# Optimization experiments

Hardware: AMD Instinct MI355X
Metric: run time of the kernel (lower is better)

Reference implementation:

```python
import jax, jax.numpy as jnp
import numpy as np

B, T, D = 4, 2048, 512
H, DK = 8, 64  # n_head, d_kv; inner_dim = H*DK = 512


def setup_inputs() -> dict:
    key = jax.random.key(0)
    ks = jax.random.split(key, 6)
    s = 1.0 / np.sqrt(D)
    return {
        "x": jax.random.normal(ks[0], (B, T, D), dtype=jnp.float32),
        "mask": jnp.zeros((B, 1, 1, T), dtype=jnp.float32),
        "position_bias": jax.random.normal(ks[1], (1, H, T, T), dtype=jnp.float32),
        "Wq": jax.random.normal(ks[2], (D, D), dtype=jnp.float32) * s,
        "Wk": jax.random.normal(ks[3], (D, D), dtype=jnp.float32) * s,
        "Wv": jax.random.normal(ks[4], (D, D), dtype=jnp.float32) * s,
        "Wo": jax.random.normal(ks[5], (D, D), dtype=jnp.float32) * s,
    }


def reference(x, mask, position_bias, Wq, Wk, Wv, Wo):
    # Linear projections (torch nn.Linear: y = x @ W.T), split into heads.
    q = (x @ Wq.T).reshape(B, T, H, DK).transpose(0, 2, 1, 3)  # [B,H,T,DK]
    k = (x @ Wk.T).reshape(B, T, H, DK).transpose(0, 2, 1, 3)  # [B,H,S,DK]
    v = (x @ Wv.T).reshape(B, T, H, DK).transpose(0, 2, 1, 3)  # [B,H,S,DK]
    # T5: no 1/sqrt(d_k) scaling; additive position bias + mask before softmax.
    scores = jnp.einsum("bhtd,bhsd->bhts", q, k) + position_bias + mask
    attn = jax.nn.softmax(scores.astype(jnp.float32), axis=-1).astype(q.dtype)
    # dropout is identity at inference
    y = jnp.einsum("bhts,bhsd->bhtd", attn, v)  # [B,H,T,DK]
    y = y.transpose(0, 2, 1, 3).reshape(B, T, H * DK)
    return y @ Wo.T
```

## Files before the change

### kernel.cpp

```cpp
#include <hip/hip_runtime.h>
#include <stdint.h>

typedef unsigned short u16;
typedef __attribute__((ext_vector_type(8))) _Float16 half8;
typedef __attribute__((ext_vector_type(4))) float f32x4;

#define L2E 1.4426950408889634f

#define NTOK 8192
#define DIM  512
#define TT   2048

__device__ __forceinline__ u16 f2h(float f) {
  _Float16 h = (_Float16)f;
  return __builtin_bit_cast(u16, h);
}

__device__ __forceinline__ void async16(const void* g, void* l) {
  __builtin_amdgcn_global_load_lds(
      (const __attribute__((address_space(1))) unsigned int*)g,
      (__attribute__((address_space(3))) unsigned int*)l, 16, 0, 0);
}

__global__ __launch_bounds__(256) void k_convert(
    const float* __restrict__ x, const float* __restrict__ wq,
    const float* __restrict__ wk, const float* __restrict__ wv,
    const float* __restrict__ wo, u16* __restrict__ xb) {
  size_t i = ((size_t)blockIdx.x * 256 + threadIdx.x) * 8;
  const float* src;
  u16* dst;
  size_t off;
  if (i < 4194304) {
    src = x; dst = xb; off = i;
  } else {
    size_t j = i - 4194304;
    int w = (int)(j >> 18);
    off = j & 262143;
    src = (w == 0) ? wq : (w == 1) ? wk : (w == 2) ? wv : wo;
    dst = xb + 4194304 + (size_t)w * 262144;
  }
  float4 a = *(const float4*)(src + off);
  float4 b = *(const float4*)(src + off + 4);
  uint4 pk;
  pk.x = (unsigned)f2h(a.x) | ((unsigned)f2h(a.y) << 16);
  pk.y = (unsigned)f2h(a.z) | ((unsigned)f2h(a.w) << 16);
  pk.z = (unsigned)f2h(b.x) | ((unsigned)f2h(b.y) << 16);
  pk.w = (unsigned)f2h(b.z) | ((unsigned)f2h(b.w) << 16);
  *(uint4*)(dst + off) = pk;
}

template <bool VSWAP>
__global__ __launch_bounds__(256) void k_proj(
    const u16* __restrict__ A, const u16* __restrict__ Wb,
    u16* __restrict__ Db) {
  const int tid = threadIdx.x;
  const int wave = tid >> 6, lane = tid & 63;
  const int quad = lane >> 4, l16 = lane & 15;
  const int wr = wave >> 1, wc = wave & 1;
  const int m0 = blockIdx.x * 128, n0 = blockIdx.y * 128;

  const u16* W;
  u16* D;
  if (VSWAP) {
    W = Wb + 2 * 262144;
    D = Db + 2 * (size_t)4194304;
  } else {
    int z = blockIdx.z;
    W = Wb + (size_t)z * 262144;
    D = Db + (size_t)z * 4194304;
  }

  __shared__ __align__(16) u16 As[128 * 64];
  __shared__ __align__(16) u16 Bs[128 * 64];

  f32x4 acc[4][4];
  for (int rt = 0; rt < 4; ++rt)
    for (int ct = 0; ct < 4; ++ct) acc[rt][ct] = (f32x4){0.f, 0.f, 0.f, 0.f};

  for (int kb = 0; kb < 8; ++kb) {
    const int k0 = kb * 64;
    for (int r = 0; r < 4; ++r) {
      int cid = r * 256 + tid;
      int row = cid >> 3, cl = cid & 7, cg = cl ^ (row & 7);
      async16(A + (size_t)(m0 + row) * DIM + k0 + cg * 8,
              &As[(r * 256 + wave * 64) * 8]);
    }
    for (int r = 0; r < 4; ++r) {
      int cid = r * 256 + tid;
      int row = cid >> 3, cl = cid & 7, cg = cl ^ (row & 7);
      async16(W + (size_t)(n0 + row) * DIM + k0 + cg * 8,
              &Bs[(r * 256 + wave * 64) * 8]);
    }
    __syncthreads();
    for (int kc = 0; kc < 2; ++kc) {
      half8 af[4], wf[4];
      for (int rt = 0; rt < 4; ++rt) {
        int row = wr * 64 + rt * 16 + l16;
        int c = (kc * 4 + quad) ^ (row & 7);
        af[rt] = *(const half8*)&As[row * 64 + c * 8];
      }
      for (int ct = 0; ct < 4; ++ct) {
        int row = wc * 64 + ct * 16 + l16;
        int c = (kc * 4 + quad) ^ (row & 7);
        wf[ct] = *(const half8*)&Bs[row * 64 + c * 8];
      }
      for (int rt = 0; rt < 4; ++rt)
        for (int ct = 0; ct < 4; ++ct)
          acc[rt][ct] = __builtin_amdgcn_mfma_f32_16x16x32_f16(
              wf[ct], af[rt], acc[rt][ct], 0, 0, 0);
    }
    __syncthreads();
  }

  for (int rt = 0; rt < 4; ++rt)
    for (int ct = 0; ct < 4; ++ct) {
      if (!VSWAP) {
        int feat0 = n0 + wc * 64 + ct * 16 + quad * 4;
        int tok   = m0 + wr * 64 + rt * 16 + l16;
        int bb = tok >> 11, t = tok & 2047, hh = feat0 >> 6, dk0 = feat0 & 63;
        uint2 pk;
        pk.x = (unsigned)f2h(acc[rt][ct][0]) |
               ((unsigned)f2h(acc[rt][ct][1]) << 16);
        pk.y = (unsigned)f2h(acc[rt][ct][2]) |
               ((unsigned)f2h(acc[rt][ct][3]) << 16);
        *(uint2*)&D[(((size_t)(bb * 8 + hh) * TT + t) << 6) + dk0] = pk;
      } else {
        for (int reg = 0; reg < 4; ++reg) {
          int feat = n0 + wc * 64 + ct * 16 + quad * 4 + reg;
          int tok  = m0 + wr * 64 + rt * 16 + l16;
          int bb = tok >> 11, t = tok & 2047, hh = feat >> 6, dk = feat & 63;
          D[(((size_t)(bb * 8 + hh) << 6) + dk) * TT + t] =
              f2h(acc[rt][ct][reg]);
        }
      }
    }
}

__global__ __launch_bounds__(256) void k_ogemm(
    const u16* __restrict__ A, const u16* __restrict__ W,
    float* __restrict__ Df) {
  const int tid = threadIdx.x;
  const int wave = tid >> 6, lane = tid & 63;
  const int quad = lane >> 4, l16 = lane & 15;
  const int wr = wave >> 1, wc = wave & 1;
  const int m0 = blockIdx.x * 64, n0 = blockIdx.y * 128;

  __shared__ __align__(16) u16 As[64 * 64];
  __shared__ __align__(16) u16 Bs[128 * 64];

  f32x4 acc[2][4];
  for (int rt = 0; rt < 2; ++rt)
    for (int ct = 0; ct < 4; ++ct) acc[rt][ct] = (f32x4){0.f, 0.f, 0.f, 0.f};

  for (int kb = 0; kb < 8; ++kb) {
    const int k0 = kb * 64;
    for (int r = 0; r < 2; ++r) {
      int cid = r * 256 + tid;
      int row = cid >> 3, cl = cid & 7, cg = cl ^ (row & 7);
      async16(A + (size_t)(m0 + row) * DIM + k0 + cg * 8,
              &As[(r * 256 + wave * 64) * 8]);
    }
    for (int r = 0; r < 4; ++r) {
      int cid = r * 256 + tid;
      int row = cid >> 3, cl = cid & 7, cg = cl ^ (row & 7);
      async16(W + (size_t)(n0 + row) * DIM + k0 + cg * 8,
              &Bs[(r * 256 + wave * 64) * 8]);
    }
    __syncthreads();
    for (int kc = 0; kc < 2; ++kc) {
      half8 af[2], wf[4];
      for (int rt = 0; rt < 2; ++rt) {
        int row = wr * 32 + rt * 16 + l16;
        int c = (kc * 4 + quad) ^ (row & 7);
        af[rt] = *(const half8*)&As[row * 64 + c * 8];
      }
      for (int ct = 0; ct < 4; ++ct) {
        int row = wc * 64 + ct * 16 + l16;
        int c = (kc * 4 + quad) ^ (row & 7);
        wf[ct] = *(const half8*)&Bs[row * 64 + c * 8];
      }
      for (int rt = 0; rt < 2; ++rt)
        for (int ct = 0; ct < 4; ++ct)
          acc[rt][ct] = __builtin_amdgcn_mfma_f32_16x16x32_f16(
              af[rt], wf[ct], acc[rt][ct], 0, 0, 0);
    }
    __syncthreads();
  }

  for (int rt = 0; rt < 2; ++rt)
    for (int ct = 0; ct < 4; ++ct)
      for (int reg = 0; reg < 4; ++reg) {
        int gm = m0 + wr * 32 + rt * 16 + quad * 4 + reg;
        int gn = n0 + wc * 64 + ct * 16 + l16;
        Df[(size_t)gm * DIM + gn] = acc[rt][ct][reg];
      }
}

__global__ __launch_bounds__(256, 4) void k_attn(
    const u16* __restrict__ Q, const u16* __restrict__ K,
    const u16* __restrict__ Vt, const float* __restrict__ bias,
    const float* __restrict__ mask, u16* __restrict__ Y) {
  const int tid = threadIdx.x;
  const int wv = tid >> 6;
  const int lane = tid & 63;
  const int quad = lane >> 4;
  const int l16 = lane & 15;

  const int bx = blockIdx.x;
  const int h = bx & 7;
  const int lid = bx >> 3;
  const int b = lid >> 5;
  const int qt = lid & 31;
  const int bh = b * 8 + h;
  const int q0 = qt * 64;

  __shared__ __align__(16) u16 Ks[128 * 64];
  __shared__ __align__(16) u16 Vs[64 * 128];
  __shared__ __align__(16) u16 Pl[64 * 64];

  const int qrow = q0 + wv * 16 + l16;
  half8 qf[2];
  {
    size_t qoff = ((size_t)bh * TT + qrow) * 64;
    qf[0] = *(const half8*)(Q + qoff + quad * 8);
    qf[1] = *(const half8*)(Q + qoff + 32 + quad * 8);
  }

  const float* brow = bias + (size_t)h * TT * TT + (size_t)qrow * TT + quad * 4;
  const float* mrow = mask + (size_t)b * TT + quad * 4;

  float m_i = -1e30f, l_i = 0.f;
  f32x4 oacc[4];
  for (int ct = 0; ct < 4; ++ct) oacc[ct] = (f32x4){0.f, 0.f, 0.f, 0.f};

  const int prow = wv * 16 + l16;
  const int r7x = (l16 & 7) << 4;
  char* plb = (char*)Pl + prow * 128;

  for (int sb = 0; sb < 16; ++sb) {
    const int s0 = sb * 128;
    for (int r = 0; r < 4; ++r) {
      int cid = r * 256 + tid;
      int row = cid >> 3, cl = cid & 7, cg = cl ^ (row & 7);
      async16(K + ((size_t)bh * TT + s0 + row) * 64 + cg * 8,
              &Ks[(r * 256 + wv * 64) * 8]);
    }
    for (int r = 0; r < 4; ++r) {
      int cid = r * 256 + tid;
      int row = cid >> 4, cl = cid & 15, cg = cl ^ (row & 7);
      async16(Vt + ((size_t)(bh * 64 + row)) * TT + s0 + cg * 8,
              &Vs[(r * 256 + wv * 64) * 8]);
    }
    f32x4 bL[8], mL[8];
    for (int ct = 0; ct < 8; ++ct) {
      bL[ct] = *(const f32x4*)(brow + s0 + ct * 16);
      mL[ct] = *(const f32x4*)(mrow + s0 + ct * 16);
    }
    __syncthreads();
    for (int ct = 0; ct < 8; ++ct) {
      bL[ct][0] += mL[ct][0]; bL[ct][1] += mL[ct][1];
      bL[ct][2] += mL[ct][2]; bL[ct][3] += mL[ct][3];
    }

#pragma unroll
    for (int hf = 0; hf < 2; ++hf) {
      f32x4 sacc[4];
      for (int ct = 0; ct < 4; ++ct) sacc[ct] = (f32x4){0.f, 0.f, 0.f, 0.f};
      __builtin_amdgcn_s_setprio(1);
      for (int kc = 0; kc < 2; ++kc) {
        half8 kf[4];
        for (int ct = 0; ct < 4; ++ct) {
          int row = hf * 64 + ct * 16 + l16;
          int c = (kc * 4 + quad) ^ (row & 7);
          kf[ct] = *(const half8*)&Ks[row * 64 + c * 8];
        }
        for (int ct = 0; ct < 4; ++ct)
          sacc[ct] = __builtin_amdgcn_mfma_f32_16x16x32_f16(kf[ct], qf[kc],
                                                            sacc[ct], 0, 0, 0);
      }
      __builtin_amdgcn_s_setprio(0);

      float sv[4][4];
      for (int ct = 0; ct < 4; ++ct)
        for (int rg = 0; rg < 4; ++rg)
          sv[ct][rg] = sacc[ct][rg] + bL[hf * 4 + ct][rg];

      float mc0 = fmaxf(fmaxf(sv[0][0], sv[0][1]), fmaxf(sv[0][2], sv[0][3]));
      float mc1 = fmaxf(fmaxf(sv[1][0], sv[1][1]), fmaxf(sv[1][2], sv[1][3]));
      float mc2 = fmaxf(fmaxf(sv[2][0], sv[2][1]), fmaxf(sv[2][2], sv[2][3]));
      float mc3 = fmaxf(fmaxf(sv[3][0], sv[3][1]), fmaxf(sv[3][2], sv[3][3]));
      float mx = fmaxf(fmaxf(mc0, mc1), fmaxf(mc2, mc3));
      mx = fmaxf(mx, __shfl_xor(mx, 16));
      mx = fmaxf(mx, __shfl_xor(mx, 32));
      float mnew = fmaxf(m_i, mx);
      float alpha = __builtin_amdgcn_exp2f((m_i - mnew) * L2E);
      float nl2e = mnew * L2E;
      float rs = 0.f;
      for (int ct = 0; ct < 4; ++ct)
        for (int rg = 0; rg < 4; ++rg) {
          float p = __builtin_amdgcn_exp2f(sv[ct][rg] * L2E - nl2e);
          sv[ct][rg] = p;
          rs += p;
        }
      rs += __shfl_xor(rs, 16);
      rs += __shfl_xor(rs, 32);
      l_i = l_i * alpha + rs;
      m_i = mnew;
      for (int ct = 0; ct < 4; ++ct) {
        oacc[ct][0] *= alpha; oacc[ct][1] *= alpha;
        oacc[ct][2] *= alpha; oacc[ct][3] *= alpha;
      }

      for (int ct = 0; ct < 4; ++ct) {
        uint2 pk;
        pk.x = (unsigned)f2h(sv[ct][0]) | ((unsigned)f2h(sv[ct][1]) << 16);
        pk.y = (unsigned)f2h(sv[ct][2]) | ((unsigned)f2h(sv[ct][3]) << 16);
        *(uint2*)(plb + ((ct * 32 + quad * 8) ^ r7x)) = pk;
      }
      asm volatile("s_waitcnt lgkmcnt(0)" ::: "memory");
      __builtin_amdgcn_sched_barrier(0);

      __builtin_amdgcn_s_setprio(1);
      for (int kc = 0; kc < 2; ++kc) {
        half8 pf = *(const half8*)(plb + ((kc * 64 + quad * 16) ^ r7x));
        half8 vf[4];
        for (int ct = 0; ct < 4; ++ct) {
          int row = ct * 16 + l16;
          int chunk = hf * 8 + ((kc * 4 + quad) ^ (row & 7));
          vf[ct] = *(const half8*)&Vs[row * 128 + chunk * 8];
        }
        for (int ct = 0; ct < 4; ++ct)
          oacc[ct] = __builtin_amdgcn_mfma_f32_16x16x32_f16(vf[ct], pf,
                                                            oacc[ct], 0, 0, 0);
      }
      __builtin_amdgcn_s_setprio(0);
    }
    __syncthreads();
  }

  float inv = 1.f / l_i;
  size_t ybase = ((size_t)(b * TT + qrow)) * DIM + h * 64 + quad * 4;
  for (int ct = 0; ct < 4; ++ct) {
    uint2 pk;
    pk.x = (unsigned)f2h(oacc[ct][0] * inv) |
           ((unsigned)f2h(oacc[ct][1] * inv) << 16);
    pk.y = (unsigned)f2h(oacc[ct][2] * inv) |
           ((unsigned)f2h(oacc[ct][3] * inv) << 16);
    *(uint2*)(Y + ybase + ct * 16) = pk;
  }
}

extern "C" void kernel_launch(void* const* d_in, const int* in_sizes, int n_in,
                              void* d_out, int out_size, void* d_ws, size_t ws_size,
                              hipStream_t stream) {
  const float* x    = (const float*)d_in[0];
  const float* mask = (const float*)d_in[1];
  const float* bias = (const float*)d_in[2];
  const float* Wq   = (const float*)d_in[3];
  const float* Wk   = (const float*)d_in[4];
  const float* Wv   = (const float*)d_in[5];
  const float* Wo   = (const float*)d_in[6];
  (void)Wk; (void)Wv;

  u16* xb  = (u16*)d_ws;
  u16* wb  = xb + 4194304;
  u16* qkv = wb + 4 * 262144;
  u16* yb  = qkv + 3 * (size_t)4194304;

  k_convert<<<2560, 256, 0, stream>>>(x, Wq, Wk, Wv, Wo, xb);
  k_proj<false><<<dim3(64, 4, 2), 256, 0, stream>>>(xb, wb, qkv);
  k_proj<true><<<dim3(64, 4), 256, 0, stream>>>(xb, wb, qkv);
  k_attn<<<1024, 256, 0, stream>>>(qkv, qkv + 4194304,
                                   qkv + 2 * (size_t)4194304, bias, mask, yb);
  k_ogemm<<<dim3(128, 4), 256, 0, stream>>>(yb, wb + 3 * 262144, (float*)d_out);
}
```

Baseline: 347.5 us.

## Double-buffer K/V tiles and prefetch position bias in attention loop

The attention kernel now iterates over 64-key tiles with two LDS buffers for K and V, issuing async loads for the next tile before computing on the current one. It also prefetches the next tile's position-bias values into registers one iteration ahead. This replaces the old scheme, which loaded 128-key tiles and waited on a barrier before every compute phase. The aim is to hide global-memory latency behind MFMA and softmax work. In exchange the loop has twice as many iterations and barriers, and dropping the min-4-blocks launch bound may let register use grow and reduce occupancy.

```diff
diff --git a/kernel.cpp b/kernel.cpp
--- a/kernel.cpp
+++ b/kernel.cpp
@@ -196,7 +196,7 @@
       }
 }
 
-__global__ __launch_bounds__(256, 4) void k_attn(
+__global__ __launch_bounds__(256) void k_attn(
     const u16* __restrict__ Q, const u16* __restrict__ K,
     const u16* __restrict__ Vt, const float* __restrict__ bias,
     const float* __restrict__ mask, u16* __restrict__ Y) {
@@ -214,8 +214,8 @@
   const int bh = b * 8 + h;
   const int q0 = qt * 64;
 
-  __shared__ __align__(16) u16 Ks[128 * 64];
-  __shared__ __align__(16) u16 Vs[64 * 128];
+  __shared__ __align__(16) u16 Ks[2][64 * 64];
+  __shared__ __align__(16) u16 Vs[2][64 * 64];
   __shared__ __align__(16) u16 Pl[64 * 64];
 
   const int qrow = q0 + wv * 16 + l16;
@@ -231,115 +231,146 @@
 
   float m_i = -1e30f, l_i = 0.f;
   f32x4 oacc[4];
+#pragma unroll
   for (int ct = 0; ct < 4; ++ct) oacc[ct] = (f32x4){0.f, 0.f, 0.f, 0.f};
 
   const int prow = wv * 16 + l16;
   const int r7x = (l16 & 7) << 4;
   char* plb = (char*)Pl + prow * 128;
 
-  for (int sb = 0; sb < 16; ++sb) {
-    const int s0 = sb * 128;
-    for (int r = 0; r < 4; ++r) {
-      int cid = r * 256 + tid;
-      int row = cid >> 3, cl = cid & 7, cg = cl ^ (row & 7);
-      async16(K + ((size_t)bh * TT + s0 + row) * 64 + cg * 8,
-              &Ks[(r * 256 + wv * 64) * 8]);
-    }
-    for (int r = 0; r < 4; ++r) {
-      int cid = r * 256 + tid;
-      int row = cid >> 4, cl = cid & 15, cg = cl ^ (row & 7);
-      async16(Vt + ((size_t)(bh * 64 + row)) * TT + s0 + cg * 8,
-              &Vs[(r * 256 + wv * 64) * 8]);
-    }
-    f32x4 bL[8], mL[8];
-    for (int ct = 0; ct < 8; ++ct) {
-      bL[ct] = *(const f32x4*)(brow + s0 + ct * 16);
+  f32x4 bL[4];
+#pragma unroll
+  for (int ct = 0; ct < 4; ++ct) bL[ct] = *(const f32x4*)(brow + ct * 16);
+  __builtin_amdgcn_sched_barrier(0);
+#pragma unroll
+  for (int r = 0; r < 2; ++r) {
+    int cid = r * 256 + tid;
+    int row = cid >> 3, cl = cid & 7, cg = cl ^ (row & 7);
+    async16(K + ((size_t)bh * TT + row) * 64 + cg * 8,
+            &Ks[0][(r * 256 + wv * 64) * 8]);
+    async16(Vt + ((size_t)(bh * 64 + row)) * TT + cg * 8,
+            &Vs[0][(r * 256 + wv * 64) * 8]);
+  }
+  __syncthreads();
+
+  for (int st = 0; st < 32; ++st) {
+    const int s0 = st * 64;
+    const int cur = st & 1;
+    const int nxt = cur ^ 1;
+
+    f32x4 mL[4], bN[4];
+    const int sn = (st < 31) ? s0 + 64 : 0;
+#pragma unroll
+    for (int ct = 0; ct < 4; ++ct) {
       mL[ct] = *(const f32x4*)(mrow + s0 + ct * 16);
-    }
-    __syncthreads();
-    for (int ct = 0; ct < 8; ++ct) {
-      bL[ct][0] += mL[ct][0]; bL[ct][1] += mL[ct][1];
-      bL[ct][2] += mL[ct][2]; bL[ct][3] += mL[ct][3];
-    }
-
-#pragma unroll
-    for (int hf = 0; hf < 2; ++hf) {
-      f32x4 sacc[4];
-      for (int ct = 0; ct < 4; ++ct) sacc[ct] = (f32x4){0.f, 0.f, 0.f, 0.f};
-      __builtin_amdgcn_s_setprio(1);
-      for (int kc = 0; kc < 2; ++kc) {
-        half8 kf[4];
-        for (int ct = 0; ct < 4; ++ct) {
-          int row = hf * 64 + ct * 16 + l16;
-          int c = (kc * 4 + quad) ^ (row & 7);
-          kf[ct] = *(const half8*)&Ks[row * 64 + c * 8];
-        }
-        for (int ct = 0; ct < 4; ++ct)
-          sacc[ct] = __builtin_amdgcn_mfma_f32_16x16x32_f16(kf[ct], qf[kc],
-                                                            sacc[ct], 0, 0, 0);
-      }
-      __builtin_amdgcn_s_setprio(0);
-
-      float sv[4][4];
+      bN[ct] = *(const f32x4*)(brow + sn + ct * 16);
+    }
+    __builtin_amdgcn_sched_barrier(0);
+
+    if (st < 31) {
+#pragma unroll
+      for (int r = 0; r < 2; ++r) {
+        int cid = r * 256 + tid;
+        int row = cid >> 3, cl = cid & 7, cg = cl ^ (row & 7);
+        async16(K + ((size_t)bh * TT + s0 + 64 + row) * 64 + cg * 8,
+                &Ks[nxt][(r * 256 + wv * 64) * 8]);
+        async16(Vt + ((size_t)(bh * 64 + row)) * TT + s0 + 64 + cg * 8,
+                &Vs[nxt][(r * 256 + wv * 64) * 8]);
+      }
+    }
+
+    f32x4 sacc[4];
+#pragma unroll
+    for (int ct = 0; ct < 4; ++ct) sacc[ct] = (f32x4){0.f, 0.f, 0.f, 0.f};
+    __builtin_amdgcn_s_setprio(1);
+#pragma unroll
+    for (int kc = 0; kc < 2; ++kc) {
+      half8 kf[4];
+#pragma unroll
+      for (int ct = 0; ct < 4; ++ct) {
+        int row = ct * 16 + l16;
+        int c = (kc * 4 + quad) ^ (row & 7);
+        kf[ct] = *(const half8*)&Ks[cur][row * 64 + c * 8];
+      }
+#pragma unroll
       for (int ct = 0; ct < 4; ++ct)
-        for (int rg = 0; rg < 4; ++rg)
-          sv[ct][rg] = sacc[ct][rg] + bL[hf * 4 + ct][rg];
-
-      float mc0 = fmaxf(fmaxf(sv[0][0], sv[0][1]), fmaxf(sv[0][2], sv[0][3]));
-      float mc1 = fmaxf(fmaxf(sv[1][0], sv[1][1]), fmaxf(sv[1][2], sv[1][3]));
-      float mc2 = fmaxf(fmaxf(sv[2][0], sv[2][1]), fmaxf(sv[2][2], sv[2][3]));
-      float mc3 = fmaxf(fmaxf(sv[3][0], sv[3][1]), fmaxf(sv[3][2], sv[3][3]));
-      float mx = fmaxf(fmaxf(mc0, mc1), fmaxf(mc2, mc3));
-      mx = fmaxf(mx, __shfl_xor(mx, 16));
-      mx = fmaxf(mx, __shfl_xor(mx, 32));
-      float mnew = fmaxf(m_i, mx);
-      float alpha = __builtin_amdgcn_exp2f((m_i - mnew) * L2E);
-      float nl2e = mnew * L2E;
-      float rs = 0.f;
+        sacc[ct] = __builtin_amdgcn_mfma_f32_16x16x32_f16(kf[ct], qf[kc],
+                                                          sacc[ct], 0, 0, 0);
+    }
+    __builtin_amdgcn_s_setprio(0);
+
+    float sv[4][4];
+#pragma unroll
+    for (int ct = 0; ct < 4; ++ct)
+#pragma unroll
+      for (int rg = 0; rg < 4; ++rg)
+        sv[ct][rg] = sacc[ct][rg] + bL[ct][rg] + mL[ct][rg];
+
+    float mc0 = fmaxf(fmaxf(sv[0][0], sv[0][1]), fmaxf(sv[0][2], sv[0][3]));
+    float mc1 = fmaxf(fmaxf(sv[1][0], sv[1][1]), fmaxf(sv[1][2], sv[1][3]));
+    float mc2 = fmaxf(fmaxf(sv[2][0], sv[2][1]), fmaxf(sv[2][2], sv[2][3]));
+    float mc3 = fmaxf(fmaxf(sv[3][0], sv[3][1]), fmaxf(sv[3][2], sv[3][3]));
+    float mx = fmaxf(fmaxf(mc0, mc1), fmaxf(mc2, mc3));
+    mx = fmaxf(mx, __shfl_xor(mx, 16));
+    mx = fmaxf(mx, __shfl_xor(mx, 32));
+    float mnew = fmaxf(m_i, mx);
+    float alpha = __builtin_amdgcn_exp2f((m_i - mnew) * L2E);
+    float nl2e = mnew * L2E;
+    float rs = 0.f;
+#pragma unroll
+    for (int ct = 0; ct < 4; ++ct)
+#pragma unroll
+      for (int rg = 0; rg < 4; ++rg) {
+        float p = __builtin_amdgcn_exp2f(sv[ct][rg] * L2E - nl2e);
+        sv[ct][rg] = p;
+        rs += p;
+      }
+    rs += __shfl_xor(rs, 16);
+    rs += __shfl_xor(rs, 32);
+    l_i = l_i * alpha + rs;
+    m_i = mnew;
+#pragma unroll
+    for (int ct = 0; ct < 4; ++ct) {
+      oacc[ct][0] *= alpha; oacc[ct][1] *= alpha;
+      oacc[ct][2] *= alpha; oacc[ct][3] *= alpha;
+    }
+
+#pragma unroll
+    for (int ct = 0; ct < 4; ++ct) {
+      uint2 pk;
+      pk.x = (unsigned)f2h(sv[ct][0]) | ((unsigned)f2h(sv[ct][1]) << 16);
+      pk.y = (unsigned)f2h(sv[ct][2]) | ((unsigned)f2h(sv[ct][3]) << 16);
+      *(uint2*)(plb + ((ct * 32 + quad * 8) ^ r7x)) = pk;
+    }
+    asm volatile("s_waitcnt lgkmcnt(0)" ::: "memory");
+    __builtin_amdgcn_sched_barrier(0);
+
+    __builtin_amdgcn_s_setprio(1);
+#pragma unroll
+    for (int kc = 0; kc < 2; ++kc) {
+      half8 pf = *(const half8*)(plb + ((kc * 64 + quad * 16) ^ r7x));
+      half8 vf[4];
+#pragma unroll
+      for (int ct = 0; ct < 4; ++ct) {
+        int row = ct * 16 + l16;
+        int c = (kc * 4 + quad) ^ (row & 7);
+        vf[ct] = *(const half8*)&Vs[cur][row * 64 + c * 8];
+      }
+#pragma unroll
       for (int ct = 0; ct < 4; ++ct)
-        for (int rg = 0; rg < 4; ++rg) {
-          float p = __builtin_amdgcn_exp2f(sv[ct][rg] * L2E - nl2e);
-          sv[ct][rg] = p;
-          rs += p;
-        }
-      rs += __shfl_xor(rs, 16);
-      rs += __shfl_xor(rs, 32);
-      l_i = l_i * alpha + rs;
-      m_i = mnew;
-      for (int ct = 0; ct < 4; ++ct) {
-        oacc[ct][0] *= alpha; oacc[ct][1] *= alpha;
-        oacc[ct][2] *= alpha; oacc[ct][3] *= alpha;
-      }
-
-      for (int ct = 0; ct < 4; ++ct) {
-        uint2 pk;
-        pk.x = (unsigned)f2h(sv[ct][0]) | ((unsigned)f2h(sv[ct][1]) << 16);
-        pk.y = (unsigned)f2h(sv[ct][2]) | ((unsigned)f2h(sv[ct][3]) << 16);
-        *(uint2*)(plb + ((ct * 32 + quad * 8) ^ r7x)) = pk;
-      }
-      asm volatile("s_waitcnt lgkmcnt(0)" ::: "memory");
-      __builtin_amdgcn_sched_barrier(0);
-
-      __builtin_amdgcn_s_setprio(1);
-      for (int kc = 0; kc < 2; ++kc) {
-        half8 pf = *(const half8*)(plb + ((kc * 64 + quad * 16) ^ r7x));
-        half8 vf[4];
-        for (int ct = 0; ct < 4; ++ct) {
-          int row = ct * 16 + l16;
-          int chunk = hf * 8 + ((kc * 4 + quad) ^ (row & 7));
-          vf[ct] = *(const half8*)&Vs[row * 128 + chunk * 8];
-        }
-        for (int ct = 0; ct < 4; ++ct)
-          oacc[ct] = __builtin_amdgcn_mfma_f32_16x16x32_f16(vf[ct], pf,
-                                                            oacc[ct], 0, 0, 0);
-      }
-      __builtin_amdgcn_s_setprio(0);
-    }
+        oacc[ct] = __builtin_amdgcn_mfma_f32_16x16x32_f16(vf[ct], pf,
+                                                          oacc[ct], 0, 0, 0);
+    }
+    __builtin_amdgcn_s_setprio(0);
+
+#pragma unroll
+    for (int ct = 0; ct < 4; ++ct) bL[ct] = bN[ct];
     __syncthreads();
   }
 
   float inv = 1.f / l_i;
   size_t ybase = ((size_t)(b * TT + qrow)) * DIM + h * 64 + quad * 4;
+#pragma unroll
   for (int ct = 0; ct < 4; ++ct) {
     uint2 pk;
     pk.x = (unsigned)f2h(oacc[ct][0] * inv) |
```

New measurement: 350.1 us. No clear change (+0.7%).
